# Kernel optimization log

Hardware: AMD Instinct MI355X
Metric: run time of the kernel (lower is better)

## Reference

```python
import jax, jax.numpy as jnp
import numpy as np

B, P, ENC = 64, 196, 2048          # batch, num_pixels (14x14), encoder_dim
A, E, D, V = 512, 512, 512, 20000  # attention_dim, embed_dim, decoder_dim, vocab
MAXLEN = 22
T = MAXLEN - 1                     # decode steps (teacher forcing drops last token)


def _lin(k, fan_in, fan_out, scale=0.02):
    return jax.random.normal(k, (fan_in, fan_out), jnp.float32) * scale, jnp.zeros((fan_out,), jnp.float32)


def setup_inputs() -> dict:
    key = jax.random.key(0)
    ks = jax.random.split(key, 16)
    encoder_out = jax.random.normal(ks[0], (B, P, ENC), jnp.float32)
    captions = jax.random.randint(ks[1], (B, MAXLEN), 0, V)
    lens = jax.random.randint(ks[2], (B,), 2, MAXLEN + 1)
    lens = jnp.sort(lens)[::-1].at[0].set(MAXLEN)  # sorted descending, as the torch loop assumes
    emb = jax.random.uniform(ks[3], (V, E), jnp.float32, -0.1, 0.1)
    enc_att_w, enc_att_b = _lin(ks[4], ENC, A)
    dec_att_w, dec_att_b = _lin(ks[5], D, A)
    full_att_w, full_att_b = _lin(ks[6], A, 1)
    w_ih = jax.random.normal(ks[7], (E + ENC, 4 * D), jnp.float32) * 0.02
    w_hh = jax.random.normal(ks[8], (D, 4 * D), jnp.float32) * 0.02
    b_ih = jnp.zeros((4 * D,), jnp.float32)
    b_hh = jnp.zeros((4 * D,), jnp.float32)
    init_h_w, init_h_b = _lin(ks[9], ENC, D)
    init_c_w, init_c_b = _lin(ks[10], ENC, D)
    f_beta_w, f_beta_b = _lin(ks[11], D, ENC)
    fc_w = jax.random.uniform(ks[12], (D, V), jnp.float32, -0.1, 0.1)
    fc_b = jnp.zeros((V,), jnp.float32)
    return dict(encoder_out=encoder_out, captions=captions, lengths=lens, emb=emb,
                enc_att_w=enc_att_w, enc_att_b=enc_att_b, dec_att_w=dec_att_w, dec_att_b=dec_att_b,
                full_att_w=full_att_w, full_att_b=full_att_b, w_ih=w_ih, b_ih=b_ih, w_hh=w_hh, b_hh=b_hh,
                init_h_w=init_h_w, init_h_b=init_h_b, init_c_w=init_c_w, init_c_b=init_c_b,
                f_beta_w=f_beta_w, f_beta_b=f_beta_b, fc_w=fc_w, fc_b=fc_b)


def reference(encoder_out, captions, lengths, emb,
              enc_att_w, enc_att_b, dec_att_w, dec_att_b, full_att_w, full_att_b,
              w_ih, b_ih, w_hh, b_hh, init_h_w, init_h_b, init_c_w, init_c_b,
              f_beta_w, f_beta_b, fc_w, fc_b):
    # Dropout is identity (eval mode) for a deterministic reference.
    dec_len = lengths - 1                       # decode_lengths
    x_emb = emb[captions]                       # (B, L, E)
    mean_enc = encoder_out.mean(axis=1)         # (B, ENC)
    h0 = mean_enc @ init_h_w + init_h_b         # (B, D)
    c0 = mean_enc @ init_c_w + init_c_b
    att1 = encoder_out @ enc_att_w + enc_att_b  # (B, P, A), hoisted out of the loop

    emb_ts = jnp.swapaxes(x_emb[:, :T, :], 0, 1)  # (T, B, E)
    t_idx = jnp.arange(T)

    def step(carry, xt):
        h, c = carry
        e_t, t = xt
        active = (t < dec_len)[:, None]         # ragged batch -> mask (sorted lengths)
        # Bahdanau attention
        att2 = h @ dec_att_w + dec_att_b        # (B, A)
        scores = (jax.nn.relu(att1 + att2[:, None, :]) @ full_att_w)[..., 0] + full_att_b[0]  # (B, P)
        alpha = jax.nn.softmax(scores, axis=1)
        context = jnp.einsum('bp,bpe->be', alpha, encoder_out)
        # gated context
        gate = jax.nn.sigmoid(h @ f_beta_w + f_beta_b)
        context = gate * context
        # LSTMCell (torch gate order i, f, g, o)
        x = jnp.concatenate([e_t, context], axis=1)
        gates = x @ w_ih + h @ w_hh + b_ih + b_hh
        i_g, f_g, g_g, o_g = jnp.split(gates, 4, axis=1)
        c_new = jax.nn.sigmoid(f_g) * c + jax.nn.sigmoid(i_g) * jnp.tanh(g_g)
        h_new = jax.nn.sigmoid(o_g) * jnp.tanh(c_new)
        h = jnp.where(active, h_new, h)
        c = jnp.where(active, c_new, c)
        preds = jnp.where(active, h_new @ fc_w + fc_b, 0.0)
        alpha_o = jnp.where(active, alpha, 0.0)
        return (h, c), (preds, alpha_o)

    _, (preds, alphas) = jax.lax.scan(step, (h0, c0), (emb_ts, t_idx))
    predictions = jnp.swapaxes(preds, 0, 1)     # (B, T, V)
    alphas = jnp.swapaxes(alphas, 0, 1)         # (B, T, P)
    return predictions, alphas
```

## Files before the change

### kernel.cpp

```cpp
#include <hip/hip_runtime.h>

#define BB   64
#define PP   196
#define ENC  2048
#define AA   512
#define EE   512
#define DD   512
#define VV   20000
#define VVP  20096
#define TT   21
#define ML   22

#define PRED_ELEMS ((size_t)BB * TT * VV)

typedef __attribute__((ext_vector_type(8))) short s8bf;
typedef __attribute__((ext_vector_type(4))) float f4acc;

__device__ __forceinline__ float bf2f(unsigned short u) {
    union { unsigned int i; float f; } v; v.i = ((unsigned int)u) << 16; return v.f;
}
__device__ __forceinline__ void unpack2(unsigned int u, float& lo, float& hi) {
    union { unsigned int i; float f; } a, b;
    a.i = u << 16; b.i = u & 0xFFFF0000u; lo = a.f; hi = b.f;
}
__device__ __forceinline__ unsigned short f2bf(float f) {
    union { float f; unsigned int i; } v; v.f = f;
    unsigned int i = v.i;
    return (unsigned short)((i + 0x7FFFu + ((i >> 16) & 1u)) >> 16);
}
__device__ __forceinline__ float sigmoidf(float x) { return 1.0f / (1.0f + __expf(-x)); }

template <bool F> __device__ __forceinline__ float ldw(const void* p, size_t i) {
    if (F) return ((const float*)p)[i];
    return bf2f(((const unsigned short*)p)[i]);
}
template <bool F> __device__ __forceinline__ unsigned short ldbf(const void* p, size_t i) {
    if (F) return f2bf(((const float*)p)[i]);
    return ((const unsigned short*)p)[i];
}
template <bool F> __device__ __forceinline__ float2 ld2(const void* p, size_t i) {
    if (F) return *(const float2*)((const float*)p + i);
    unsigned int u = *(const unsigned int*)((const unsigned short*)p + i);
    float lo, hi; unpack2(u, lo, hi); return make_float2(lo, hi);
}
template <bool F> __device__ __forceinline__ float4 ld4(const void* p, size_t i) {
    if (F) return *(const float4*)((const float*)p + i);
    uint2 u = *(const uint2*)((const unsigned short*)p + i);
    float a, b, c, d; unpack2(u.x, a, b); unpack2(u.y, c, d);
    return make_float4(a, b, c, d);
}
template <bool F> __device__ __forceinline__ void st1(void* p, size_t i, float v) {
    if (F) ((float*)p)[i] = v; else ((unsigned short*)p)[i] = f2bf(v);
}

__global__ void dec_detect_kernel(const unsigned short* __restrict__ enc_us, int* __restrict__ flag) {
    __shared__ int s_cnt;
    if (threadIdx.x == 0) s_cnt = 0;
    __syncthreads();
    int cnt = 0;
    for (int i = threadIdx.x; i < 8192; i += 256) {
        unsigned short u = enc_us[2 * i];
        if ((u & 0x7F80) == 0x7F80) cnt++;
    }
    if (cnt) atomicAdd(&s_cnt, cnt);
    __syncthreads();
    if (threadIdx.x == 0) *flag = (s_cnt > 0) ? 1 : 0;
}

template <bool F>
__device__ __forceinline__ void conv_swz_body(const void* W, int K, int Norig,
                                              unsigned short* dst, int permMode, int nChunks) {
    int chunk = blockIdx.x * 4 + (threadIdx.x >> 6);
    if (chunk >= nChunks) return;
    int lane = threadIdx.x & 63;
    int KC = K >> 5;
    int nt = chunk / KC, kc = chunk % KC;
    int quad = lane >> 4, l15 = lane & 15;
    int np = nt * 16 + l15;
    int col;
    if (permMode == 1) col = ((np >> 5) & 3) * 512 + (np >> 7) * 32 + (np & 31);
    else col = np;
    union { s8bf v; unsigned short s[8]; } o;
    if (np < Norig || permMode == 1) {
        size_t base = (size_t)(kc * 32 + quad * 8) * Norig + col;
#pragma unroll
        for (int j = 0; j < 8; ++j) o.s[j] = ldbf<F>(W, base + (size_t)j * Norig);
    } else {
#pragma unroll
        for (int j = 0; j < 8; ++j) o.s[j] = 0;
    }
    *(s8bf*)(dst + ((size_t)chunk * 64 + lane) * 8) = o.v;
}
__global__ void conv_swz_kernel(const int* __restrict__ flg, const void* __restrict__ W,
                                int K, int Norig, unsigned short* __restrict__ dst,
                                int permMode, int nChunks) {
    if (*flg) conv_swz_body<true>(W, K, Norig, dst, permMode, nChunks);
    else      conv_swz_body<false>(W, K, Norig, dst, permMode, nChunks);
}

template <bool F>
__device__ __forceinline__ void conv_bias_body(const void* dab, const void* fbb,
                                               const void* bih, const void* bhh, const void* fcb,
                                               const void* ihb, const void* icb, const void* eab,
                                               float* ag_b, float* g_b, float* fc_b,
                                               float* ihb_f, float* icb_f, float* eab_f) {
    int i = blockIdx.x * 256 + threadIdx.x;
    if (i < 2560) ag_b[i] = (i < 512) ? ldw<F>(dab, i) : ldw<F>(fbb, i - 512);
    else if (i < 2560 + 2048) {
        int np = i - 2560;
        int orig = ((np >> 5) & 3) * 512 + (np >> 7) * 32 + (np & 31);
        g_b[np] = ldw<F>(bih, orig) + ldw<F>(bhh, orig);
    } else if (i < 2560 + 2048 + 20000) fc_b[i - 4608] = ldw<F>(fcb, i - 4608);
    else if (i < 2560 + 2048 + 20000 + 512) ihb_f[i - 24608] = ldw<F>(ihb, i - 24608);
    else if (i < 2560 + 2048 + 20000 + 1024) icb_f[i - 25120] = ldw<F>(icb, i - 25120);
    else if (i < 2560 + 2048 + 20000 + 1536) eab_f[i - 25632] = ldw<F>(eab, i - 25632);
}
__global__ void conv_bias_kernel(const int* __restrict__ flg,
                                 const void* dab, const void* fbb, const void* bih, const void* bhh,
                                 const void* fcb, const void* ihb, const void* icb, const void* eab,
                                 float* ag_b, float* g_b, float* fc_b,
                                 float* ihb_f, float* icb_f, float* eab_f) {
    if (*flg) conv_bias_body<true>(dab, fbb, bih, bhh, fcb, ihb, icb, eab, ag_b, g_b, fc_b, ihb_f, icb_f, eab_f);
    else      conv_bias_body<false>(dab, fbb, bih, bhh, fcb, ihb, icb, eab, ag_b, g_b, fc_b, ihb_f, icb_f, eab_f);
}

template <bool F>
__device__ __forceinline__ void mean_body(const void* enc, unsigned short* mean_bf) {
    int b = blockIdx.x;
    int e = blockIdx.y * 256 + threadIdx.x;
    size_t base = (size_t)b * PP * ENC + e;
    float s = 0.f;
#pragma unroll 4
    for (int p = 0; p < PP; ++p) s += ldw<F>(enc, base + (size_t)p * ENC);
    mean_bf[b * ENC + e] = f2bf(s * (1.0f / (float)PP));
}
__global__ void dec_mean_kernel(const void* __restrict__ enc, const int* __restrict__ flg,
                                unsigned short* __restrict__ mean_bf) {
    if (*flg) mean_body<true>(enc, mean_bf); else mean_body<false>(enc, mean_bf);
}

__global__ __launch_bounds__(256)
void gemm_u_kernel(const int* __restrict__ flg,
                   const unsigned short* __restrict__ A1, int K1, const unsigned short* __restrict__ W1,
                   const unsigned short* __restrict__ A2, int K2, const unsigned short* __restrict__ W2,
                   const float* __restrict__ bias, int N, int epi,
                   float* __restrict__ outF, float* __restrict__ outF2,
                   unsigned short* __restrict__ hb, float* __restrict__ cptr,
                   void* __restrict__ outV, const int* __restrict__ lengths, int t) {
    __shared__ float s_g[4 * 64 * 32];
    int tid = threadIdx.x;
    int wave = tid >> 6, lane = tid & 63;
    int l15 = lane & 15, quad = lane >> 4;
    f4acc acc[4][2];
#pragma unroll
    for (int a = 0; a < 4; ++a) { acc[a][0] = (f4acc)0.f; acc[a][1] = (f4acc)0.f; }
#pragma unroll
    for (int pass = 0; pass < 2; ++pass) {
        const unsigned short* A = pass ? A2 : A1;
        if (!A) continue;
        int K = pass ? K2 : K1;
        const unsigned short* W = pass ? W2 : W1;
        int KC = K >> 5;
        for (int kc = 0; kc < KC; ++kc) {
            s8bf af[4];
#pragma unroll
            for (int rt = 0; rt < 4; ++rt)
                af[rt] = *(const s8bf*)(A + (size_t)(rt * 16 + l15) * K + kc * 32 + quad * 8);
#pragma unroll
            for (int ct = 0; ct < 2; ++ct) {
                int nt = blockIdx.y * 8 + ct * 4 + wave;
                s8bf bv = *(const s8bf*)(W + ((size_t)(nt * KC + kc) * 64 + lane) * 8);
#pragma unroll
                for (int rt = 0; rt < 4; ++rt)
                    acc[rt][ct] = __builtin_amdgcn_mfma_f32_16x16x32_bf16(af[rt], bv, acc[rt][ct], 0, 0, 0);
            }
        }
    }
    if (epi == 4) {
#pragma unroll
        for (int ct = 0; ct < 2; ++ct) {
            int nl = wave * 16 + ct * 64 + l15;
            int g = nl >> 5, dl = nl & 31;
            float bv = bias[blockIdx.y * 128 + nl];
#pragma unroll
            for (int rt = 0; rt < 4; ++rt)
#pragma unroll
                for (int r = 0; r < 4; ++r) {
                    int m = rt * 16 + quad * 4 + r;
                    s_g[(g * 64 + m) * 32 + dl] = acc[rt][ct][r] + bv;
                }
        }
        __syncthreads();
        int m = tid >> 2;
        bool act = t < (lengths[m] - 1);
        if (act) {
#pragma unroll
            for (int i = 0; i < 8; ++i) {
                int dl = (tid & 3) * 8 + i;
                int d = blockIdx.y * 32 + dl;
                float ig = sigmoidf(s_g[(0 * 64 + m) * 32 + dl]);
                float fg = sigmoidf(s_g[(1 * 64 + m) * 32 + dl]);
                float gg = tanhf(s_g[(2 * 64 + m) * 32 + dl]);
                float og = sigmoidf(s_g[(3 * 64 + m) * 32 + dl]);
                float cn = fg * cptr[m * DD + d] + ig * gg;
                float hn = og * tanhf(cn);
                cptr[m * DD + d] = cn;
                hb[m * DD + d] = f2bf(hn);
            }
        }
        return;
    }
    bool f32o = (epi == 2) ? (*flg != 0) : false;
#pragma unroll
    for (int ct = 0; ct < 2; ++ct) {
        int n = blockIdx.y * 128 + ct * 64 + wave * 16 + l15;
        if (n >= N) continue;
        float bv = bias ? bias[n] : 0.f;
#pragma unroll
        for (int rt = 0; rt < 4; ++rt)
#pragma unroll
            for (int r = 0; r < 4; ++r) {
                int m = rt * 16 + quad * 4 + r;
                float v = acc[rt][ct][r] + bv;
                if (epi == 0)      outF[(size_t)m * N + n] = v;
                else if (epi == 1) {
                    if (n < 512) outF[(size_t)m * 512 + n] = v;
                    else         outF2[(size_t)m * 2048 + (n - 512)] = sigmoidf(v);
                } else if (epi == 3) hb[(size_t)m * DD + n] = f2bf(v);
                else {
                    bool act = t < (lengths[m] - 1);
                    float pv = act ? v : 0.f;
                    size_t oi = ((size_t)m * TT + t) * VV + n;
                    if (f32o) ((float*)outV)[oi] = pv; else ((unsigned short*)outV)[oi] = f2bf(pv);
                }
            }
    }
}

template <bool F>
__device__ __forceinline__ void att1_gemm_body(const void* enc, const unsigned short* Wsw,
                                               const float* bias, float* att1) {
    __shared__ __attribute__((aligned(16))) unsigned short As[64 * 40];
    int tid = threadIdx.x;
    int wave = tid >> 6, lane = tid & 63;
    int l15 = lane & 15, quad = lane >> 4;
    int row0 = blockIdx.x * 64;
    f4acc acc[4][2];
#pragma unroll
    for (int a = 0; a < 4; ++a) { acc[a][0] = (f4acc)0.f; acc[a][1] = (f4acc)0.f; }
    int lr = tid >> 2, lk = (tid & 3) * 8;
    for (int kc = 0; kc < 64; ++kc) {
        int k0 = kc * 32;
        if (F) {
            const float* src = (const float*)enc + (size_t)(row0 + lr) * ENC + k0 + lk;
            float4 v0 = *(const float4*)src, v1 = *(const float4*)(src + 4);
            union { s8bf v; unsigned short s[8]; } t8;
            t8.s[0]=f2bf(v0.x); t8.s[1]=f2bf(v0.y); t8.s[2]=f2bf(v0.z); t8.s[3]=f2bf(v0.w);
            t8.s[4]=f2bf(v1.x); t8.s[5]=f2bf(v1.y); t8.s[6]=f2bf(v1.z); t8.s[7]=f2bf(v1.w);
            *(s8bf*)&As[lr * 40 + lk] = t8.v;
        } else {
            *(s8bf*)&As[lr * 40 + lk] =
                *(const s8bf*)((const unsigned short*)enc + (size_t)(row0 + lr) * ENC + k0 + lk);
        }
        __syncthreads();
        s8bf af[4];
#pragma unroll
        for (int rt = 0; rt < 4; ++rt)
            af[rt] = *(const s8bf*)&As[(rt * 16 + l15) * 40 + quad * 8];
#pragma unroll
        for (int ct = 0; ct < 2; ++ct) {
            int nt = blockIdx.y * 8 + ct * 4 + wave;
            s8bf bv = *(const s8bf*)(Wsw + ((size_t)(nt * 64 + kc) * 64 + lane) * 8);
#pragma unroll
            for (int rt = 0; rt < 4; ++rt)
                acc[rt][ct] = __builtin_amdgcn_mfma_f32_16x16x32_bf16(af[rt], bv, acc[rt][ct], 0, 0, 0);
        }
        __syncthreads();
    }
#pragma unroll
    for (int ct = 0; ct < 2; ++ct) {
        int n = blockIdx.y * 128 + ct * 64 + wave * 16 + l15;
        float bv = bias[n];
#pragma unroll
        for (int rt = 0; rt < 4; ++rt)
#pragma unroll
            for (int r = 0; r < 4; ++r) {
                int m = row0 + rt * 16 + quad * 4 + r;
                att1[(size_t)m * AA + n] = acc[rt][ct][r] + bv;
            }
    }
}
__global__ __launch_bounds__(256)
void gemm_att1_kernel(const void* __restrict__ enc, const int* __restrict__ flg,
                      const unsigned short* __restrict__ Wsw, const float* __restrict__ bias,
                      float* __restrict__ att1) {
    if (*flg) att1_gemm_body<true>(enc, Wsw, bias, att1);
    else      att1_gemm_body<false>(enc, Wsw, bias, att1);
}

template <bool F>
__device__ __forceinline__ void att_body(const float* att1, const float* att2,
                                         const void* faw, const void* fab,
                                         const int* lengths, float* alpha_ws, void* out, int t) {
    __shared__ float s_att2[AA];
    __shared__ float s_fw[AA];
    __shared__ float s_red[256];
    int b = blockIdx.x, tid = threadIdx.x;
    for (int a = tid; a < AA; a += 256) { s_att2[a] = att2[b * AA + a]; s_fw[a] = ldw<F>(faw, a); }
    __syncthreads();
    float sc = -1e30f;
    if (tid < PP) {
        const float4* r = (const float4*)(att1 + (size_t)(b * PP + tid) * AA);
        float acc = 0.f;
#pragma unroll 4
        for (int a4 = 0; a4 < AA / 4; ++a4) {
            float4 v = r[a4];
            int a = a4 * 4;
            acc += fmaxf(v.x + s_att2[a], 0.f)     * s_fw[a]
                 + fmaxf(v.y + s_att2[a + 1], 0.f) * s_fw[a + 1]
                 + fmaxf(v.z + s_att2[a + 2], 0.f) * s_fw[a + 2]
                 + fmaxf(v.w + s_att2[a + 3], 0.f) * s_fw[a + 3];
        }
        sc = acc + ldw<F>(fab, 0);
    }
    s_red[tid] = sc;
    __syncthreads();
    for (int s = 128; s > 0; s >>= 1) { if (tid < s) s_red[tid] = fmaxf(s_red[tid], s_red[tid + s]); __syncthreads(); }
    float m = s_red[0];
    __syncthreads();
    float e = 0.f;
    if (tid < PP) e = __expf(sc - m);
    s_red[tid] = e;
    __syncthreads();
    for (int s = 128; s > 0; s >>= 1) { if (tid < s) s_red[tid] += s_red[tid + s]; __syncthreads(); }
    float inv = 1.0f / s_red[0];
    if (tid < PP) {
        float al = e * inv;
        alpha_ws[b * PP + tid] = al;
        bool active = t < (lengths[b] - 1);
        st1<F>(out, PRED_ELEMS + (size_t)(b * TT + t) * PP + tid, active ? al : 0.f);
    }
}
__global__ void dec_att_kernel(const float* __restrict__ att1, const float* __restrict__ att2,
                               const int* __restrict__ flg,
                               const void* __restrict__ faw, const void* __restrict__ fab,
                               const int* __restrict__ lengths,
                               float* __restrict__ alpha_ws, void* __restrict__ out, int t) {
    if (*flg) att_body<true>(att1, att2, faw, fab, lengths, alpha_ws, out, t);
    else      att_body<false>(att1, att2, faw, fab, lengths, alpha_ws, out, t);
}

template <bool F>
__device__ __forceinline__ void ctx_partial_body(const void* enc, const float* alpha_ws, float* partial) {
    __shared__ float s_al[PP];
    int b = blockIdx.x, half = blockIdx.y, pc = blockIdx.z, tid = threadIdx.x;
    if (tid < PP) s_al[tid] = alpha_ws[b * PP + tid];
    __syncthreads();
    int e = half * 1024 + tid * 4;
    float a0 = 0.f, a1 = 0.f, a2 = 0.f, a3 = 0.f;
    int p0 = pc * 49;
#pragma unroll 4
    for (int p = p0; p < p0 + 49; ++p) {
        float al = s_al[p];
        float4 v = ld4<F>(enc, (size_t)(b * PP + p) * ENC + e);
        a0 += al * v.x; a1 += al * v.y; a2 += al * v.z; a3 += al * v.w;
    }
    *(float4*)&partial[(size_t)(b * 4 + pc) * ENC + e] = make_float4(a0, a1, a2, a3);
}
__global__ void dec_ctx_partial_kernel(const void* __restrict__ enc, const int* __restrict__ flg,
                                       const float* __restrict__ alpha_ws, float* __restrict__ partial) {
    if (*flg) ctx_partial_body<true>(enc, alpha_ws, partial);
    else      ctx_partial_body<false>(enc, alpha_ws, partial);
}

template <bool F>
__device__ __forceinline__ void ctx_reduce_body(const float* partial, const float* gate,
                                                const void* emb, const int* captions,
                                                unsigned short* x_bf, int t) {
    int b = blockIdx.x, half = blockIdx.y, tid = threadIdx.x;
    if (half == 0) {
        int cap = captions[b * ML + t];
        int i = tid * 2;
        float2 ev = ld2<F>(emb, (size_t)cap * EE + i);
        *(unsigned int*)(x_bf + (size_t)b * 2560 + i) =
            (unsigned int)f2bf(ev.x) | ((unsigned int)f2bf(ev.y) << 16);
    }
    int e = half * 1024 + tid * 4;
    float4 s = *(const float4*)&partial[(size_t)(b * 4 + 0) * ENC + e];
#pragma unroll
    for (int pc = 1; pc < 4; ++pc) {
        float4 v = *(const float4*)&partial[(size_t)(b * 4 + pc) * ENC + e];
        s.x += v.x; s.y += v.y; s.z += v.z; s.w += v.w;
    }
    float4 g = *(const float4*)&gate[(size_t)b * ENC + e];
    uint2 pk;
    pk.x = (unsigned int)f2bf(s.x * g.x) | ((unsigned int)f2bf(s.y * g.y) << 16);
    pk.y = (unsigned int)f2bf(s.z * g.z) | ((unsigned int)f2bf(s.w * g.w) << 16);
    *(uint2*)(x_bf + (size_t)b * 2560 + EE + e) = pk;
}
__global__ void dec_ctx_reduce_kernel(const float* __restrict__ partial, const float* __restrict__ gate,
                                      const int* __restrict__ flg,
                                      const void* __restrict__ emb, const int* __restrict__ captions,
                                      unsigned short* __restrict__ x_bf, int t) {
    if (*flg) ctx_reduce_body<true>(partial, gate, emb, captions, x_bf, t);
    else      ctx_reduce_body<false>(partial, gate, emb, captions, x_bf, t);
}

extern "C" void kernel_launch(void* const* d_in, const int* in_sizes, int n_in,
                              void* d_out, int out_size, void* d_ws, size_t ws_size,
                              hipStream_t stream) {
    const void* enc      = d_in[0];
    const int* captions  = (const int*)d_in[1];
    const int* lengths   = (const int*)d_in[2];
    const void* emb      = d_in[3];
    const void* eaw      = d_in[4];
    const void* eab      = d_in[5];
    const void* daw      = d_in[6];
    const void* dab      = d_in[7];
    const void* faw      = d_in[8];
    const void* fab      = d_in[9];
    const void* wih      = d_in[10];
    const void* bih      = d_in[11];
    const void* whh      = d_in[12];
    const void* bhh      = d_in[13];
    const void* ihw      = d_in[14];
    const void* ihb      = d_in[15];
    const void* icw      = d_in[16];
    const void* icb      = d_in[17];
    const void* fbw      = d_in[18];
    const void* fbb      = d_in[19];
    const void* fcw      = d_in[20];
    const void* fcb      = d_in[21];

    char* cur = (char*)d_ws;
    auto alloc = [&](size_t bytes) { void* p = cur; cur += (bytes + 255) & ~(size_t)255; return p; };
    int* flg               = (int*)alloc(4);
    unsigned short* h_bf   = (unsigned short*)alloc((size_t)BB * DD * 2);
    unsigned short* x_bf   = (unsigned short*)alloc((size_t)BB * 2560 * 2);
    unsigned short* mean_bf= (unsigned short*)alloc((size_t)BB * ENC * 2);
    float* c               = (float*)alloc((size_t)BB * DD * 4);
    float* att2            = (float*)alloc((size_t)BB * AA * 4);
    float* gate            = (float*)alloc((size_t)BB * ENC * 4);
    float* alpha           = (float*)alloc((size_t)BB * PP * 4);
    float* partial         = (float*)alloc((size_t)BB * 4 * ENC * 4);
    float* ag_bias         = (float*)alloc(2560 * 4);
    float* g_bias          = (float*)alloc(2048 * 4);
    float* fc_bias         = (float*)alloc(20000 * 4);
    float* ihb_f           = (float*)alloc(512 * 4);
    float* icb_f           = (float*)alloc(512 * 4);
    float* eab_f           = (float*)alloc(512 * 4);
    unsigned short* eaw_sw = (unsigned short*)alloc((size_t)32 * 64 * 512 * 2);
    unsigned short* ag_sw  = (unsigned short*)alloc((size_t)160 * 16 * 512 * 2);
    unsigned short* ihw_sw = (unsigned short*)alloc((size_t)32 * 64 * 512 * 2);
    unsigned short* icw_sw = (unsigned short*)alloc((size_t)32 * 64 * 512 * 2);
    unsigned short* wih_sw = (unsigned short*)alloc((size_t)128 * 80 * 512 * 2);
    unsigned short* whh_sw = (unsigned short*)alloc((size_t)128 * 16 * 512 * 2);
    unsigned short* fcw_sw = (unsigned short*)alloc((size_t)1256 * 16 * 512 * 2);
    float* att1            = (float*)alloc((size_t)BB * PP * AA * 4);

    dec_detect_kernel<<<1, 256, 0, stream>>>((const unsigned short*)enc, flg);
    conv_swz_kernel<<<(32 * 64 + 3) / 4, 256, 0, stream>>>(flg, eaw, ENC, AA, eaw_sw, 0, 32 * 64);
    conv_swz_kernel<<<(32 * 16 + 3) / 4, 256, 0, stream>>>(flg, daw, DD, AA, ag_sw, 0, 32 * 16);
    conv_swz_kernel<<<(128 * 16 + 3) / 4, 256, 0, stream>>>(flg, fbw, DD, ENC, ag_sw + (size_t)32 * 16 * 512, 0, 128 * 16);
    conv_swz_kernel<<<(32 * 64 + 3) / 4, 256, 0, stream>>>(flg, ihw, ENC, DD, ihw_sw, 0, 32 * 64);
    conv_swz_kernel<<<(32 * 64 + 3) / 4, 256, 0, stream>>>(flg, icw, ENC, DD, icw_sw, 0, 32 * 64);
    conv_swz_kernel<<<(128 * 80 + 3) / 4, 256, 0, stream>>>(flg, wih, 2560, 2048, wih_sw, 1, 128 * 80);
    conv_swz_kernel<<<(128 * 16 + 3) / 4, 256, 0, stream>>>(flg, whh, DD, 2048, whh_sw, 1, 128 * 16);
    conv_swz_kernel<<<(1256 * 16 + 3) / 4, 256, 0, stream>>>(flg, fcw, DD, VV, fcw_sw, 0, 1256 * 16);
    conv_bias_kernel<<<(26144 + 255) / 256, 256, 0, stream>>>(flg, dab, fbb, bih, bhh, fcb, ihb, icb, eab,
                                                              ag_bias, g_bias, fc_bias, ihb_f, icb_f, eab_f);
    dec_mean_kernel<<<dim3(BB, ENC / 256), 256, 0, stream>>>(enc, flg, mean_bf);
    gemm_u_kernel<<<dim3(1, 4), 256, 0, stream>>>(flg, mean_bf, ENC, ihw_sw, nullptr, 0, nullptr,
                                                  ihb_f, DD, 3, nullptr, nullptr, h_bf, nullptr, nullptr, nullptr, 0);
    gemm_u_kernel<<<dim3(1, 4), 256, 0, stream>>>(flg, mean_bf, ENC, icw_sw, nullptr, 0, nullptr,
                                                  icb_f, DD, 0, c, nullptr, nullptr, nullptr, nullptr, nullptr, 0);
    gemm_att1_kernel<<<dim3(196, 4), 256, 0, stream>>>(enc, flg, eaw_sw, eab_f, att1);

    for (int t = 0; t < TT; ++t) {
        gemm_u_kernel<<<dim3(1, 20), 256, 0, stream>>>(flg, h_bf, DD, ag_sw, nullptr, 0, nullptr,
                                                       ag_bias, 2560, 1, att2, gate, nullptr, nullptr, nullptr, nullptr, 0);
        dec_att_kernel<<<BB, 256, 0, stream>>>(att1, att2, flg, faw, fab, lengths, alpha, d_out, t);
        dec_ctx_partial_kernel<<<dim3(BB, 2, 4), 256, 0, stream>>>(enc, flg, alpha, partial);
        dec_ctx_reduce_kernel<<<dim3(BB, 2), 256, 0, stream>>>(partial, gate, flg, emb, captions, x_bf, t);
        gemm_u_kernel<<<dim3(1, 16), 256, 0, stream>>>(flg, x_bf, 2560, wih_sw, h_bf, DD, whh_sw,
                                                       g_bias, 2048, 4, nullptr, nullptr, h_bf, c, nullptr, lengths, t);
        gemm_u_kernel<<<dim3(1, 157), 256, 0, stream>>>(flg, h_bf, DD, fcw_sw, nullptr, 0, nullptr,
                                                        fc_bias, VV, 2, nullptr, nullptr, nullptr, nullptr, d_out, lengths, t);
    }
}
```

Baseline: 3.140 ms.

## Batch vocab projection after the recurrence and narrow recurrent GEMM tiles

Each step's hidden state is stored into an h_all buffer, and one large fc GEMM runs over all 21 steps after the loop, instead of 21 small launches inside it. The hidden state is double-buffered, since the LSTM GEMM now reads the old h while writing the new one. The per-step GEMMs use one column tile per block, giving 2x more blocks for better CU occupancy. The attention-score kernel now uses wave-per-row shuffle reductions, and the context partial and reduce kernels are fused into one. This cuts serial-chain length and launch count, at the cost of extra h_all storage and a longer per-thread reduction over all 196 pixels in the context kernel.

```diff
diff --git a/kernel.cpp b/kernel.cpp
--- a/kernel.cpp
+++ b/kernel.cpp
@@ -7,7 +7,6 @@
 #define EE   512
 #define DD   512
 #define VV   20000
-#define VVP  20096
 #define TT   21
 #define ML   22
 
@@ -78,7 +77,7 @@
     int quad = lane >> 4, l15 = lane & 15;
     int np = nt * 16 + l15;
     int col;
-    if (permMode == 1) col = ((np >> 5) & 3) * 512 + (np >> 7) * 32 + (np & 31);
+    if (permMode == 1) col = ((np >> 4) & 3) * 512 + (np >> 6) * 16 + (np & 15);
     else col = np;
     union { s8bf v; unsigned short s[8]; } o;
     if (np < Norig || permMode == 1) {
@@ -108,7 +107,7 @@
     if (i < 2560) ag_b[i] = (i < 512) ? ldw<F>(dab, i) : ldw<F>(fbb, i - 512);
     else if (i < 2560 + 2048) {
         int np = i - 2560;
-        int orig = ((np >> 5) & 3) * 512 + (np >> 7) * 32 + (np & 31);
+        int orig = ((np >> 4) & 3) * 512 + (np >> 6) * 16 + (np & 15);
         g_b[np] = ldw<F>(bih, orig) + ldw<F>(bhh, orig);
     } else if (i < 2560 + 2048 + 20000) fc_b[i - 4608] = ldw<F>(fcb, i - 4608);
     else if (i < 2560 + 2048 + 20000 + 512) ihb_f[i - 24608] = ldw<F>(ihb, i - 24608);
@@ -143,20 +142,23 @@
 void gemm_u_kernel(const int* __restrict__ flg,
                    const unsigned short* __restrict__ A1, int K1, const unsigned short* __restrict__ W1,
                    const unsigned short* __restrict__ A2, int K2, const unsigned short* __restrict__ W2,
-                   const float* __restrict__ bias, int N, int epi,
+                   const float* __restrict__ bias, int N, int epi, int nct,
                    float* __restrict__ outF, float* __restrict__ outF2,
                    unsigned short* __restrict__ hb, float* __restrict__ cptr,
+                   unsigned short* __restrict__ h_all,
                    void* __restrict__ outV, const int* __restrict__ lengths, int t) {
-    __shared__ float s_g[4 * 64 * 32];
+    __shared__ float s_g[4 * 64 * 17];
     int tid = threadIdx.x;
     int wave = tid >> 6, lane = tid & 63;
     int l15 = lane & 15, quad = lane >> 4;
+    const unsigned short* Abase1 = A1;
+    if (epi == 2) Abase1 = A1 + (size_t)blockIdx.x * 64 * K1;
     f4acc acc[4][2];
 #pragma unroll
     for (int a = 0; a < 4; ++a) { acc[a][0] = (f4acc)0.f; acc[a][1] = (f4acc)0.f; }
 #pragma unroll
     for (int pass = 0; pass < 2; ++pass) {
-        const unsigned short* A = pass ? A2 : A1;
+        const unsigned short* A = pass ? A2 : Abase1;
         if (!A) continue;
         int K = pass ? K2 : K1;
         const unsigned short* W = pass ? W2 : W1;
@@ -167,8 +169,8 @@
             for (int rt = 0; rt < 4; ++rt)
                 af[rt] = *(const s8bf*)(A + (size_t)(rt * 16 + l15) * K + kc * 32 + quad * 8);
 #pragma unroll
-            for (int ct = 0; ct < 2; ++ct) {
-                int nt = blockIdx.y * 8 + ct * 4 + wave;
+            for (int ct = 0; ct < 2; ++ct) if (ct < nct) {
+                int nt = blockIdx.y * 4 * nct + ct * 4 + wave;
                 s8bf bv = *(const s8bf*)(W + ((size_t)(nt * KC + kc) * 64 + lane) * 8);
 #pragma unroll
                 for (int rt = 0; rt < 4; ++rt)
@@ -177,43 +179,46 @@
         }
     }
     if (epi == 4) {
-#pragma unroll
-        for (int ct = 0; ct < 2; ++ct) {
-            int nl = wave * 16 + ct * 64 + l15;
-            int g = nl >> 5, dl = nl & 31;
-            float bv = bias[blockIdx.y * 128 + nl];
-#pragma unroll
-            for (int rt = 0; rt < 4; ++rt)
-#pragma unroll
-                for (int r = 0; r < 4; ++r) {
-                    int m = rt * 16 + quad * 4 + r;
-                    s_g[(g * 64 + m) * 32 + dl] = acc[rt][ct][r] + bv;
-                }
-        }
+        int nl = wave * 16 + l15;
+        int g = (nl >> 4) & 3, dl = nl & 15;
+        float bv = bias[blockIdx.y * 64 + nl];
+#pragma unroll
+        for (int rt = 0; rt < 4; ++rt)
+#pragma unroll
+            for (int r = 0; r < 4; ++r) {
+                int m = rt * 16 + quad * 4 + r;
+                s_g[(g * 64 + m) * 17 + dl] = acc[rt][0][r] + bv;
+            }
         __syncthreads();
         int m = tid >> 2;
         bool act = t < (lengths[m] - 1);
-        if (act) {
-#pragma unroll
-            for (int i = 0; i < 8; ++i) {
-                int dl = (tid & 3) * 8 + i;
-                int d = blockIdx.y * 32 + dl;
-                float ig = sigmoidf(s_g[(0 * 64 + m) * 32 + dl]);
-                float fg = sigmoidf(s_g[(1 * 64 + m) * 32 + dl]);
-                float gg = tanhf(s_g[(2 * 64 + m) * 32 + dl]);
-                float og = sigmoidf(s_g[(3 * 64 + m) * 32 + dl]);
+#pragma unroll
+        for (int i = 0; i < 4; ++i) {
+            int dl2 = (tid & 3) * 4 + i;
+            int d = blockIdx.y * 16 + dl2;
+            unsigned short hv;
+            if (act) {
+                float ig = sigmoidf(s_g[(0 * 64 + m) * 17 + dl2]);
+                float fg = sigmoidf(s_g[(1 * 64 + m) * 17 + dl2]);
+                float gg = tanhf(s_g[(2 * 64 + m) * 17 + dl2]);
+                float og = sigmoidf(s_g[(3 * 64 + m) * 17 + dl2]);
                 float cn = fg * cptr[m * DD + d] + ig * gg;
                 float hn = og * tanhf(cn);
                 cptr[m * DD + d] = cn;
-                hb[m * DD + d] = f2bf(hn);
+                hv = f2bf(hn);
+            } else {
+                hv = A2[(size_t)m * K2 + d];
             }
+            hb[m * DD + d] = hv;
+            h_all[((size_t)t * BB + m) * DD + d] = hv;
         }
         return;
     }
     bool f32o = (epi == 2) ? (*flg != 0) : false;
-#pragma unroll
-    for (int ct = 0; ct < 2; ++ct) {
-        int n = blockIdx.y * 128 + ct * 64 + wave * 16 + l15;
+    int tb = blockIdx.x;
+#pragma unroll
+    for (int ct = 0; ct < 2; ++ct) if (ct < nct) {
+        int n = blockIdx.y * 64 * nct + ct * 64 + wave * 16 + l15;
         if (n >= N) continue;
         float bv = bias ? bias[n] : 0.f;
 #pragma unroll
@@ -228,9 +233,9 @@
                     else         outF2[(size_t)m * 2048 + (n - 512)] = sigmoidf(v);
                 } else if (epi == 3) hb[(size_t)m * DD + n] = f2bf(v);
                 else {
-                    bool act = t < (lengths[m] - 1);
+                    bool act = tb < (lengths[m] - 1);
                     float pv = act ? v : 0.f;
-                    size_t oi = ((size_t)m * TT + t) * VV + n;
+                    size_t oi = ((size_t)m * TT + tb) * VV + n;
                     if (f32o) ((float*)outV)[oi] = pv; else ((unsigned short*)outV)[oi] = f2bf(pv);
                 }
             }
@@ -302,27 +307,37 @@
 __device__ __forceinline__ void att_body(const float* att1, const float* att2,
                                          const void* faw, const void* fab,
                                          const int* lengths, float* alpha_ws, void* out, int t) {
-    __shared__ float s_att2[AA];
-    __shared__ float s_fw[AA];
+    __shared__ float s_sc[256];
     __shared__ float s_red[256];
     int b = blockIdx.x, tid = threadIdx.x;
-    for (int a = tid; a < AA; a += 256) { s_att2[a] = att2[b * AA + a]; s_fw[a] = ldw<F>(faw, a); }
-    __syncthreads();
-    float sc = -1e30f;
-    if (tid < PP) {
-        const float4* r = (const float4*)(att1 + (size_t)(b * PP + tid) * AA);
-        float acc = 0.f;
-#pragma unroll 4
-        for (int a4 = 0; a4 < AA / 4; ++a4) {
-            float4 v = r[a4];
-            int a = a4 * 4;
-            acc += fmaxf(v.x + s_att2[a], 0.f)     * s_fw[a]
-                 + fmaxf(v.y + s_att2[a + 1], 0.f) * s_fw[a + 1]
-                 + fmaxf(v.z + s_att2[a + 2], 0.f) * s_fw[a + 2]
-                 + fmaxf(v.w + s_att2[a + 3], 0.f) * s_fw[a + 3];
-        }
-        sc = acc + ldw<F>(fab, 0);
-    }
+    int wave = tid >> 6, lane = tid & 63;
+    int a0i = lane * 8;
+    float4 a2a = *(const float4*)(att2 + (size_t)b * AA + a0i);
+    float4 a2b = *(const float4*)(att2 + (size_t)b * AA + a0i + 4);
+    float4 w0 = ld4<F>(faw, a0i);
+    float4 w1 = ld4<F>(faw, a0i + 4);
+    float fabv = ldw<F>(fab, 0);
+    s_sc[tid] = -1e30f;
+    __syncthreads();
+#pragma unroll 2
+    for (int r = wave; r < PP; r += 4) {
+        const float4* row = (const float4*)(att1 + ((size_t)b * PP + r) * AA);
+        float4 v0 = row[lane * 2];
+        float4 v1 = row[lane * 2 + 1];
+        float acc = fmaxf(v0.x + a2a.x, 0.f) * w0.x
+                  + fmaxf(v0.y + a2a.y, 0.f) * w0.y
+                  + fmaxf(v0.z + a2a.z, 0.f) * w0.z
+                  + fmaxf(v0.w + a2a.w, 0.f) * w0.w
+                  + fmaxf(v1.x + a2b.x, 0.f) * w1.x
+                  + fmaxf(v1.y + a2b.y, 0.f) * w1.y
+                  + fmaxf(v1.z + a2b.z, 0.f) * w1.z
+                  + fmaxf(v1.w + a2b.w, 0.f) * w1.w;
+#pragma unroll
+        for (int off = 32; off; off >>= 1) acc += __shfl_xor(acc, off, 64);
+        if (lane == 0) s_sc[r] = acc + fabv;
+    }
+    __syncthreads();
+    float sc = s_sc[tid];
     s_red[tid] = sc;
     __syncthreads();
     for (int s = 128; s > 0; s >>= 1) { if (tid < s) s_red[tid] = fmaxf(s_red[tid], s_red[tid + s]); __syncthreads(); }
@@ -351,59 +366,39 @@
 }
 
 template <bool F>
-__device__ __forceinline__ void ctx_partial_body(const void* enc, const float* alpha_ws, float* partial) {
+__device__ __forceinline__ void ctx_body(const void* enc, const float* alpha_ws, const float* gate,
+                                         const void* emb, const int* captions,
+                                         unsigned short* x_bf, int t) {
     __shared__ float s_al[PP];
-    int b = blockIdx.x, half = blockIdx.y, pc = blockIdx.z, tid = threadIdx.x;
+    int b = blockIdx.x, yc = blockIdx.y, tid = threadIdx.x;
     if (tid < PP) s_al[tid] = alpha_ws[b * PP + tid];
     __syncthreads();
-    int e = half * 1024 + tid * 4;
-    float a0 = 0.f, a1 = 0.f, a2 = 0.f, a3 = 0.f;
-    int p0 = pc * 49;
-#pragma unroll 4
-    for (int p = p0; p < p0 + 49; ++p) {
-        float al = s_al[p];
-        float4 v = ld4<F>(enc, (size_t)(b * PP + p) * ENC + e);
-        a0 += al * v.x; a1 += al * v.y; a2 += al * v.z; a3 += al * v.w;
-    }
-    *(float4*)&partial[(size_t)(b * 4 + pc) * ENC + e] = make_float4(a0, a1, a2, a3);
-}
-__global__ void dec_ctx_partial_kernel(const void* __restrict__ enc, const int* __restrict__ flg,
-                                       const float* __restrict__ alpha_ws, float* __restrict__ partial) {
-    if (*flg) ctx_partial_body<true>(enc, alpha_ws, partial);
-    else      ctx_partial_body<false>(enc, alpha_ws, partial);
-}
-
-template <bool F>
-__device__ __forceinline__ void ctx_reduce_body(const float* partial, const float* gate,
-                                                const void* emb, const int* captions,
-                                                unsigned short* x_bf, int t) {
-    int b = blockIdx.x, half = blockIdx.y, tid = threadIdx.x;
-    if (half == 0) {
+    if (yc == 0) {
         int cap = captions[b * ML + t];
         int i = tid * 2;
         float2 ev = ld2<F>(emb, (size_t)cap * EE + i);
         *(unsigned int*)(x_bf + (size_t)b * 2560 + i) =
             (unsigned int)f2bf(ev.x) | ((unsigned int)f2bf(ev.y) << 16);
     }
-    int e = half * 1024 + tid * 4;
-    float4 s = *(const float4*)&partial[(size_t)(b * 4 + 0) * ENC + e];
-#pragma unroll
-    for (int pc = 1; pc < 4; ++pc) {
-        float4 v = *(const float4*)&partial[(size_t)(b * 4 + pc) * ENC + e];
-        s.x += v.x; s.y += v.y; s.z += v.z; s.w += v.w;
-    }
-    float4 g = *(const float4*)&gate[(size_t)b * ENC + e];
-    uint2 pk;
-    pk.x = (unsigned int)f2bf(s.x * g.x) | ((unsigned int)f2bf(s.y * g.y) << 16);
-    pk.y = (unsigned int)f2bf(s.z * g.z) | ((unsigned int)f2bf(s.w * g.w) << 16);
-    *(uint2*)(x_bf + (size_t)b * 2560 + EE + e) = pk;
-}
-__global__ void dec_ctx_reduce_kernel(const float* __restrict__ partial, const float* __restrict__ gate,
-                                      const int* __restrict__ flg,
-                                      const void* __restrict__ emb, const int* __restrict__ captions,
-                                      unsigned short* __restrict__ x_bf, int t) {
-    if (*flg) ctx_reduce_body<true>(partial, gate, emb, captions, x_bf, t);
-    else      ctx_reduce_body<false>(partial, gate, emb, captions, x_bf, t);
+    int e = yc * 512 + tid * 2;
+    float a0 = 0.f, a1 = 0.f;
+    size_t base = (size_t)b * PP * ENC + e;
+#pragma unroll 4
+    for (int p = 0; p < PP; ++p) {
+        float al = s_al[p];
+        float2 v = ld2<F>(enc, base + (size_t)p * ENC);
+        a0 += al * v.x; a1 += al * v.y;
+    }
+    float2 g = *(const float2*)&gate[(size_t)b * ENC + e];
+    *(unsigned int*)(x_bf + (size_t)b * 2560 + EE + e) =
+        (unsigned int)f2bf(a0 * g.x) | ((unsigned int)f2bf(a1 * g.y) << 16);
+}
+__global__ void dec_ctx_kernel(const void* __restrict__ enc, const int* __restrict__ flg,
+                               const float* __restrict__ alpha_ws, const float* __restrict__ gate,
+                               const void* __restrict__ emb, const int* __restrict__ captions,
+                               unsigned short* __restrict__ x_bf, int t) {
+    if (*flg) ctx_body<true>(enc, alpha_ws, gate, emb, captions, x_bf, t);
+    else      ctx_body<false>(enc, alpha_ws, gate, emb, captions, x_bf, t);
 }
 
 extern "C" void kernel_launch(void* const* d_in, const int* in_sizes, int n_in,
@@ -435,14 +430,15 @@
     char* cur = (char*)d_ws;
     auto alloc = [&](size_t bytes) { void* p = cur; cur += (bytes + 255) & ~(size_t)255; return p; };
     int* flg               = (int*)alloc(4);
-    unsigned short* h_bf   = (unsigned short*)alloc((size_t)BB * DD * 2);
+    unsigned short* h_bufA = (unsigned short*)alloc((size_t)BB * DD * 2);
+    unsigned short* h_bufB = (unsigned short*)alloc((size_t)BB * DD * 2);
+    unsigned short* h_all  = (unsigned short*)alloc((size_t)TT * BB * DD * 2);
     unsigned short* x_bf   = (unsigned short*)alloc((size_t)BB * 2560 * 2);
     unsigned short* mean_bf= (unsigned short*)alloc((size_t)BB * ENC * 2);
     float* c               = (float*)alloc((size_t)BB * DD * 4);
     float* att2            = (float*)alloc((size_t)BB * AA * 4);
     float* gate            = (float*)alloc((size_t)BB * ENC * 4);
     float* alpha           = (float*)alloc((size_t)BB * PP * 4);
-    float* partial         = (float*)alloc((size_t)BB * 4 * ENC * 4);
     float* ag_bias         = (float*)alloc(2560 * 4);
     float* g_bias          = (float*)alloc(2048 * 4);
     float* fc_bias         = (float*)alloc(20000 * 4);
@@ -471,20 +467,27 @@
                                                               ag_bias, g_bias, fc_bias, ihb_f, icb_f, eab_f);
     dec_mean_kernel<<<dim3(BB, ENC / 256), 256, 0, stream>>>(enc, flg, mean_bf);
     gemm_u_kernel<<<dim3(1, 4), 256, 0, stream>>>(flg, mean_bf, ENC, ihw_sw, nullptr, 0, nullptr,
-                                                  ihb_f, DD, 3, nullptr, nullptr, h_bf, nullptr, nullptr, nullptr, 0);
+                                                  ihb_f, DD, 3, 2, nullptr, nullptr, h_bufA, nullptr,
+                                                  nullptr, nullptr, nullptr, 0);
     gemm_u_kernel<<<dim3(1, 4), 256, 0, stream>>>(flg, mean_bf, ENC, icw_sw, nullptr, 0, nullptr,
-                                                  icb_f, DD, 0, c, nullptr, nullptr, nullptr, nullptr, nullptr, 0);
+                                                  icb_f, DD, 0, 2, c, nullptr, nullptr, nullptr,
+                                                  nullptr, nullptr, nullptr, 0);
     gemm_att1_kernel<<<dim3(196, 4), 256, 0, stream>>>(enc, flg, eaw_sw, eab_f, att1);
 
+    unsigned short* hcur = h_bufA;
     for (int t = 0; t < TT; ++t) {
-        gemm_u_kernel<<<dim3(1, 20), 256, 0, stream>>>(flg, h_bf, DD, ag_sw, nullptr, 0, nullptr,
-                                                       ag_bias, 2560, 1, att2, gate, nullptr, nullptr, nullptr, nullptr, 0);
+        unsigned short* hnext = (hcur == h_bufA) ? h_bufB : h_bufA;
+        gemm_u_kernel<<<dim3(1, 40), 256, 0, stream>>>(flg, hcur, DD, ag_sw, nullptr, 0, nullptr,
+                                                       ag_bias, 2560, 1, 1, att2, gate, nullptr, nullptr,
+                                                       nullptr, nullptr, nullptr, 0);
         dec_att_kernel<<<BB, 256, 0, stream>>>(att1, att2, flg, faw, fab, lengths, alpha, d_out, t);
-        dec_ctx_partial_kernel<<<dim3(BB, 2, 4), 256, 0, stream>>>(enc, flg, alpha, partial);
-        dec_ctx_reduce_kernel<<<dim3(BB, 2), 256, 0, stream>>>(partial, gate, flg, emb, captions, x_bf, t);
-        gemm_u_kernel<<<dim3(1, 16), 256, 0, stream>>>(flg, x_bf, 2560, wih_sw, h_bf, DD, whh_sw,
-                                                       g_bias, 2048, 4, nullptr, nullptr, h_bf, c, nullptr, lengths, t);
-        gemm_u_kernel<<<dim3(1, 157), 256, 0, stream>>>(flg, h_bf, DD, fcw_sw, nullptr, 0, nullptr,
-                                                        fc_bias, VV, 2, nullptr, nullptr, nullptr, nullptr, d_out, lengths, t);
-    }
-}
+        dec_ctx_kernel<<<dim3(BB, 4), 256, 0, stream>>>(enc, flg, alpha, gate, emb, captions, x_bf, t);
+        gemm_u_kernel<<<dim3(1, 32), 256, 0, stream>>>(flg, x_bf, 2560, wih_sw, hcur, DD, whh_sw,
+                                                       g_bias, 2048, 4, 1, nullptr, nullptr, hnext, c,
+                                                       h_all, nullptr, lengths, t);
+        hcur = hnext;
+    }
+    gemm_u_kernel<<<dim3(TT, 157), 256, 0, stream>>>(flg, h_all, DD, fcw_sw, nullptr, 0, nullptr,
+                                                     fc_bias, VV, 2, 2, nullptr, nullptr, nullptr, nullptr,
+                                                     nullptr, d_out, lengths, 0);
+}
```

Result: no change. 3.098 ms (-1.3%).
